# Optimization experiments

Measured on AMD Instinct MI355X. Metric: run time of the kernel, lower is better.

The kernel has to match this reference:

```python
import jax, jax.numpy as jnp
import numpy as np

B, P, N = 64, 100, 1000
D, H, QD = 128, 8, 16
NUM_PATCHES = 196
NTOT = N + NUM_PATCHES
SQRT_D = float(np.sqrt(D))   # sqrt_embedding_dim
CLIP = 10.0                  # logit_clipping


def setup_inputs() -> dict:
    key = jax.random.key(0)
    ks = jax.random.split(key, 10)
    return {
        "encoded_last_node": jax.random.normal(ks[0], (B, P, D), jnp.float32),
        "ninf_mask": jnp.zeros((B, P, N), jnp.float32),
        "q_first": jax.random.normal(ks[1], (B, H, P, QD), jnp.float32),
        "k": jax.random.normal(ks[2], (B, H, NTOT, QD), jnp.float32),
        "v": jax.random.normal(ks[3], (B, H, NTOT, QD), jnp.float32),
        "single_head_key": jax.random.normal(ks[4], (B, D, N), jnp.float32),
        "Wq_last": jax.random.normal(ks[5], (D, H * QD), jnp.float32) * 0.05,
        "mh_combine": jax.random.normal(ks[6], (H * QD, D), jnp.float32) * 0.05,
        "edge_bias": jax.random.normal(ks[7], (B, N, N), jnp.float32) * 0.1,
        "current_node": jax.random.randint(ks[8], (B, P), 0, N, jnp.int64),
        "num_patches": NUM_PATCHES,
    }


def reference(encoded_last_node, ninf_mask, q_first, k, v, single_head_key,
              Wq_last, mh_combine, edge_bias, current_node, num_patches):
    b, p, _ = encoded_last_node.shape
    h, qd = q_first.shape[1], q_first.shape[3]

    # q_last = reshape_by_heads(F.linear(x, Wq_last_para))  -> [B,H,P,qd]
    q_last = (encoded_last_node @ Wq_last.T).reshape(b, p, h, qd).transpose(0, 2, 1, 3)
    q = q_first + q_last

    # multi-head attention with mask extended by zero columns for patch tokens
    mask_full = jnp.pad(ninf_mask, ((0, 0), (0, 0), (0, num_patches)))  # [B,P,Ntot]
    score = jnp.einsum('bhpd,bhnd->bhpn', q, k) / jnp.sqrt(jnp.float32(qd))
    weights = jax.nn.softmax(score + mask_full[:, None, :, :], axis=-1)
    out = jnp.einsum('bhpn,bhnd->bhpd', weights, v)
    out_concat = out.transpose(0, 2, 1, 3).reshape(b, p, h * qd)  # [B,P,D]

    mh_atten_out = out_concat @ mh_combine.T                       # [B,P,D]

    # pointer-style single-head score with tanh clipping
    score2 = jnp.einsum('bpd,bdn->bpn', mh_atten_out, single_head_key)
    score_clipped = CLIP * jnp.tanh(score2 / SQRT_D)

    # gather edge bias row for current node: bias[b,p,n] = edge_bias[b, current_node[b,p], n]
    bias_row = jnp.take_along_axis(edge_bias, current_node[:, :, None], axis=1)
    probs = jax.nn.softmax(score_clipped + bias_row + ninf_mask, axis=-1)
    return probs
```

## Files before the change

kernel.cpp:

```cpp
#include <hip/hip_runtime.h>
#include <math.h>

#define BB 64
#define PP 100
#define NN 1000
#define DD 128
#define HH 8
#define QDQ 16
#define NTOT 1196
#define QROWS 16
#define LOG2E 1.44269504088896f
#define EXP2(x) __builtin_amdgcn_exp2f(x)

typedef float f2 __attribute__((ext_vector_type(2)));
typedef short s8v __attribute__((ext_vector_type(8)));
typedef float f16v __attribute__((ext_vector_type(16)));

static __device__ __forceinline__ f2 splat2(float v) { f2 r; r.x = v; r.y = v; return r; }
#define PKFMA(a, b, c) __builtin_elementwise_fma((a), (b), (c))

static __device__ __forceinline__ unsigned pkhi(float a, float b) {
  return (__float_as_uint(a) >> 16) | (__float_as_uint(b) & 0xffff0000u);
}
static __device__ __forceinline__ float truncbf(float a) {
  return __uint_as_float(__float_as_uint(a) & 0xffff0000u);
}
#define MFMA32(a, b, c) __builtin_amdgcn_mfma_f32_32x32x16_bf16((a), (b), (c), 0, 0, 0)

__global__ __launch_bounds__(256) void k_prep(const float* __restrict__ x,
                                              const float* __restrict__ Wq,
                                              const float* __restrict__ qf,
                                              float* __restrict__ qout,
                                              const float* __restrict__ mask,
                                              unsigned short* __restrict__ m2) {
  __shared__ float sw[128 * 65];
  __shared__ float xs[QROWS * DD];
  int tid = threadIdx.x;

  if (blockIdx.x < 400) {
    int row0 = blockIdx.x * QROWS;
    for (int i = tid; i < QROWS * DD / 4; i += 256)
      ((float4*)xs)[i] = ((const float4*)(x + (size_t)row0 * DD))[i];

    int j = tid & 127, rr = tid >> 7;
    float acc[8];
#pragma unroll
    for (int i = 0; i < 8; ++i) acc[i] = 0.f;

    for (int half = 0; half < 2; ++half) {
      __syncthreads();
      for (int idx = tid; idx < 128 * 64; idx += 256) {
        int jj = idx >> 6, dl = idx & 63;
        sw[jj * 65 + dl] = Wq[jj * DD + half * 64 + dl];
      }
      __syncthreads();
#pragma unroll
      for (int ri = 0; ri < 8; ++ri) {
        int r = 2 * ri + rr;
        float a = acc[ri];
#pragma unroll 16
        for (int dl = 0; dl < 64; ++dl)
          a += xs[r * DD + half * 64 + dl] * sw[j * 65 + dl];
        acc[ri] = a;
      }
    }
#pragma unroll
    for (int ri = 0; ri < 8; ++ri) {
      int bp = row0 + 2 * ri + rr;
      int b = bp / PP, p = bp % PP;
      int h = j >> 4, qd = j & 15;
      size_t qi = ((size_t)(b * HH + h) * PP + p) * QDQ + qd;
      qout[qi] = acc[ri] + qf[qi];
    }
  } else {
    int t2 = blockIdx.x - 400;
    int b = t2 >> 7, q = t2 & 127;
    unsigned short* dst = m2 + (size_t)(b * 128 + q) * 1280;
    const float* srow = mask + ((size_t)b * PP + (q < PP ? q : PP - 1)) * NN;
    for (int j = tid; j < 1280; j += 256) {
      int h = j >= 640 ? 1 : 0;
      int jj = j - h * 640;
      float val;
      if (q >= PP || jj >= 598) {
        val = -1e4f;
      } else {
        int n = h * 598 + jj;
        val = (n < NN) ? srow[n] * LOG2E - 20.f : -20.f;
      }
      dst[j] = (unsigned short)(__float_as_uint(val) >> 16);
    }
  }
}

__global__ __launch_bounds__(256) void k_mha(const float* __restrict__ kk,
                                             const float* __restrict__ vv,
                                             const float* __restrict__ qws,
                                             const unsigned short* __restrict__ m2,
                                             float* __restrict__ part) {
  int bid = blockIdx.x;
  int swz = (bid & 7) * 128 + (bid >> 3);
  int bh = swz >> 1, half = swz & 1;
  int b = bh >> 3;
  int tid = threadIdx.x;
  int w = tid >> 6, lane = tid & 63;
  int L = lane >> 5, ln = lane & 31;
  bool lo = (L == 0);

  __shared__ __align__(16) char pool[27264];
  char* KspB = pool;
  char* VThB = pool + 10240;
  char* VTlB = pool + 14592;
  char* QhB  = pool + 18944;
  char* QlB  = pool + 23040;

  {
    const float* qrow = qws + (size_t)bh * (PP * QDQ);
    for (int i = tid; i < 128 * 16; i += 256) {
      int p = i >> 4, qd = i & 15;
      float v = (p < PP) ? qrow[p * QDQ + qd] * (0.25f * LOG2E) : 0.f;
      ((unsigned short*)QhB)[i] = (unsigned short)(__float_as_uint(v) >> 16);
      float rl = v - truncbf(v);
      ((unsigned short*)QlB)[i] = (unsigned short)(__float_as_uint(rl) >> 16);
    }
  }

  const float4* kf4 = (const float4*)kk + (size_t)bh * NTOT * 4;
  const float4* vf4 = (const float4*)vv + (size_t)bh * NTOT * 4;

  f16v Oacc[4];
  float lacc[4];
#pragma unroll
  for (int qt = 0; qt < 4; ++qt) {
    lacc[qt] = 0.f;
#pragma unroll
    for (int r = 0; r < 16; ++r) Oacc[qt][r] = 0.f;
  }
  s8v QhF[4], QlF[4];

  for (int c = 0; c < 5; ++c) {
    __syncthreads();
#pragma unroll
    for (int rep = 0; rep < 2; ++rep) {
      int f = tid + rep * 256;
      int key_l = f >> 2, qd0 = (f & 3) << 2;
      int j = c * 128 + key_l;
      int jc = j < 598 ? j : 597;
      size_t gidx = (size_t)(half * 598 + jc) * 4 + (qd0 >> 2);
      float4 k4 = kf4[gidx];
      unsigned kh01 = pkhi(k4.x, k4.y), kh23 = pkhi(k4.z, k4.w);
      float r0 = k4.x - truncbf(k4.x), r1 = k4.y - truncbf(k4.y);
      float r2 = k4.z - truncbf(k4.z), r3 = k4.w - truncbf(k4.w);
      unsigned kl01 = pkhi(r0, r1), kl23 = pkhi(r2, r3);
      *(uint2*)(KspB + key_l * 80 + qd0 * 2) = make_uint2(kh01, kh23);
      *(uint2*)(KspB + key_l * 80 + 32 + qd0 * 2) = make_uint2(kl01, kl23);
      float4 v4 = vf4[gidx];
      float ve0 = v4.x, ve1 = v4.y, ve2 = v4.z, ve3 = v4.w;
      ((unsigned short*)VThB)[(qd0 + 0) * 136 + key_l] = (unsigned short)(__float_as_uint(ve0) >> 16);
      ((unsigned short*)VThB)[(qd0 + 1) * 136 + key_l] = (unsigned short)(__float_as_uint(ve1) >> 16);
      ((unsigned short*)VThB)[(qd0 + 2) * 136 + key_l] = (unsigned short)(__float_as_uint(ve2) >> 16);
      ((unsigned short*)VThB)[(qd0 + 3) * 136 + key_l] = (unsigned short)(__float_as_uint(ve3) >> 16);
      float w0 = ve0 - truncbf(ve0), w1 = ve1 - truncbf(ve1);
      float w2 = ve2 - truncbf(ve2), w3 = ve3 - truncbf(ve3);
      ((unsigned short*)VTlB)[(qd0 + 0) * 136 + key_l] = (unsigned short)(__float_as_uint(w0) >> 16);
      ((unsigned short*)VTlB)[(qd0 + 1) * 136 + key_l] = (unsigned short)(__float_as_uint(w1) >> 16);
      ((unsigned short*)VTlB)[(qd0 + 2) * 136 + key_l] = (unsigned short)(__float_as_uint(w2) >> 16);
      ((unsigned short*)VTlB)[(qd0 + 3) * 136 + key_l] = (unsigned short)(__float_as_uint(w3) >> 16);
    }
    __syncthreads();
    if (c == 0) {
#pragma unroll
      for (int qt = 0; qt < 4; ++qt) {
        int qr = qt * 32 + ln;
        QhF[qt] = *(const s8v*)(QhB + qr * 32 + L * 16);
        QlF[qt] = *(const s8v*)(QlB + qr * 32 + L * 16);
      }
    }
    int ktb = w * 32;
    s8v KhF = *(const s8v*)(KspB + (ktb + ln) * 80 + L * 16);
    s8v KlF = *(const s8v*)(KspB + (ktb + ln) * 80 + 32 + L * 16);
    int vr = ln & 15;
    s8v VhS0 = *(const s8v*)(VThB + vr * 272 + (ktb + L * 8) * 2);
    s8v VhS1 = *(const s8v*)(VThB + vr * 272 + (ktb + 16 + L * 8) * 2);
    s8v VlS0 = *(const s8v*)(VTlB + vr * 272 + (ktb + L * 8) * 2);
    s8v VlS1 = *(const s8v*)(VTlB + vr * 272 + (ktb + 16 + L * 8) * 2);
    size_t mkey = (size_t)half * 640 + c * 128 + ktb + 4 * L;
#pragma unroll
    for (int qt = 0; qt < 4; ++qt) {
      const unsigned short* mrow = m2 + (size_t)(b * 128 + qt * 32 + ln) * 1280 + mkey;
      f16v acc;
#pragma unroll
      for (int g = 0; g < 4; ++g) {
        uint2 md = *(const uint2*)(mrow + g * 8);
        acc[g * 4 + 0] = __uint_as_float(md.x << 16);
        acc[g * 4 + 1] = __uint_as_float(md.x & 0xffff0000u);
        acc[g * 4 + 2] = __uint_as_float(md.y << 16);
        acc[g * 4 + 3] = __uint_as_float(md.y & 0xffff0000u);
      }
      acc = MFMA32(KhF, QhF[qt], acc);
      acc = MFMA32(KhF, QlF[qt], acc);
      acc = MFMA32(KlF, QhF[qt], acc);
      float p[16];
      float ls = 0.f;
#pragma unroll
      for (int r = 0; r < 16; ++r) { p[r] = EXP2(acc[r]); ls += p[r]; }
      lacc[qt] += ls;
#pragma unroll
      for (int s = 0; s < 2; ++s) {
        unsigned a0 = pkhi(p[8 * s + 0], p[8 * s + 1]), a1 = pkhi(p[8 * s + 2], p[8 * s + 3]);
        unsigned b0 = pkhi(p[8 * s + 4], p[8 * s + 5]), b1 = pkhi(p[8 * s + 6], p[8 * s + 7]);
        unsigned m0 = lo ? b0 : a0;
        unsigned m1 = lo ? b1 : a1;
        unsigned s0 = __shfl_xor(m0, 32);
        unsigned s1 = __shfl_xor(m1, 32);
        uint4 phu = make_uint4(lo ? a0 : s0, lo ? a1 : s1, lo ? s0 : b0, lo ? s1 : b1);
        float t0 = p[8 * s + 0] - truncbf(p[8 * s + 0]), t1 = p[8 * s + 1] - truncbf(p[8 * s + 1]);
        float t2 = p[8 * s + 2] - truncbf(p[8 * s + 2]), t3 = p[8 * s + 3] - truncbf(p[8 * s + 3]);
        float t4 = p[8 * s + 4] - truncbf(p[8 * s + 4]), t5 = p[8 * s + 5] - truncbf(p[8 * s + 5]);
        float t6 = p[8 * s + 6] - truncbf(p[8 * s + 6]), t7 = p[8 * s + 7] - truncbf(p[8 * s + 7]);
        unsigned c0 = pkhi(t0, t1), c1 = pkhi(t2, t3);
        unsigned e0 = pkhi(t4, t5), e1 = pkhi(t6, t7);
        unsigned n0 = lo ? e0 : c0;
        unsigned n1 = lo ? e1 : c1;
        unsigned u0 = __shfl_xor(n0, 32);
        unsigned u1 = __shfl_xor(n1, 32);
        uint4 plu = make_uint4(lo ? c0 : u0, lo ? c1 : u1, lo ? u0 : e0, lo ? u1 : e1);
        s8v APh = *(s8v*)&phu;
        s8v APl = *(s8v*)&plu;
        s8v Vh = s ? VhS1 : VhS0;
        s8v Vl = s ? VlS1 : VlS0;
        Oacc[qt] = MFMA32(APh, Vh, Oacc[qt]);
        Oacc[qt] = MFMA32(APh, Vl, Oacc[qt]);
        Oacc[qt] = MFMA32(APl, Vh, Oacc[qt]);
      }
    }
  }

  float lf[4];
#pragma unroll
  for (int qt = 0; qt < 4; ++qt) lf[qt] = lacc[qt] + __shfl_xor(lacc[qt], 32);

  __syncthreads();
  float* marea = (float*)pool;
  float* larea = (float*)(pool + 25600);
  if (ln < 16) {
#pragma unroll
    for (int qt = 0; qt < 4; ++qt) {
#pragma unroll
      for (int r = 0; r < 16; ++r) {
        int q = qt * 32 + (r & 3) + 8 * (r >> 2) + 4 * L;
        if (q < PP) marea[(w * PP + q) * 16 + ln] = Oacc[qt][r];
      }
    }
  }
  if (lane < 32) {
#pragma unroll
    for (int qt = 0; qt < 4; ++qt) {
      int q = qt * 32 + ln;
      if (q < PP) larea[w * PP + q] = lf[qt];
    }
  }
  __syncthreads();
  for (int idx = tid; idx < PP * 17; idx += 256) {
    int q = idx / 17, e = idx % 17;
    float sv;
    if (e < 16)
      sv = marea[(0 * PP + q) * 16 + e] + marea[(1 * PP + q) * 16 + e]
         + marea[(2 * PP + q) * 16 + e] + marea[(3 * PP + q) * 16 + e];
    else
      sv = larea[0 * PP + q] + larea[1 * PP + q] + larea[2 * PP + q] + larea[3 * PP + q];
    part[((size_t)swz * PP + q) * 17 + e] = sv;
  }
}

__global__ __launch_bounds__(256) void k_combine(const float* __restrict__ part,
                                                 const float* __restrict__ MC,
                                                 float* __restrict__ mh) {
  __shared__ float sw[128 * 65];
  __shared__ float oc[QROWS * DD];
  int tid = threadIdx.x;
  int row0 = blockIdx.x * QROWS;

  for (int i = tid; i < QROWS * DD; i += 256) {
    int r = i >> 7, t = i & 127;
    int bp = row0 + r, b = bp / PP, p = bp % PP;
    int qd = t & 15, h = t >> 4;
    int bh = b * HH + h;
    const float* r0 = part + (((size_t)(bh * 2 + 0)) * PP + p) * 17;
    const float* r1 = part + (((size_t)(bh * 2 + 1)) * PP + p) * 17;
    float A = r0[qd] + r1[qd];
    float L = r0[16] + r1[16];
    oc[i] = A / L;
  }

  int j = tid & 127, rr = tid >> 7;
  float acc[8];
#pragma unroll
  for (int i = 0; i < 8; ++i) acc[i] = 0.f;

  for (int half = 0; half < 2; ++half) {
    __syncthreads();
    for (int idx = tid; idx < 128 * 64; idx += 256) {
      int jj = idx >> 6, dl = idx & 63;
      sw[jj * 65 + dl] = MC[jj * DD + half * 64 + dl];
    }
    __syncthreads();
#pragma unroll
    for (int ri = 0; ri < 8; ++ri) {
      int r = 2 * ri + rr;
      float a = acc[ri];
#pragma unroll 16
      for (int dl = 0; dl < 64; ++dl)
        a += oc[r * DD + half * 64 + dl] * sw[j * 65 + dl];
      acc[ri] = a;
    }
  }
#pragma unroll
  for (int ri = 0; ri < 8; ++ri) {
    int bp = row0 + 2 * ri + rr;
    mh[(size_t)bp * DD + j] = acc[ri];
  }
}

__global__ __launch_bounds__(256) void k_score2(const float* __restrict__ mh,
                                                const float* __restrict__ shk,
                                                float* __restrict__ sc) {
  int bid = blockIdx.x;
  int swz = (bid & 7) * 128 + (bid >> 3);
  int b = swz >> 4, nt = swz & 15;
  int tid = threadIdx.x; int nl = tid & 31, pg = tid >> 5;
  __shared__ float A[PP * 132];
  for (int idx = tid; idx < PP * DD; idx += 256)
    A[(idx >> 7) * 132 + (idx & 127)] = mh[(size_t)b * PP * DD + idx];
  __syncthreads();

  int na = nt * 64 + nl, nb2 = na + 32;
  int nca = na < NN ? na : NN - 1, ncb = nb2 < NN ? nb2 : NN - 1;
  const float* S = shk + (size_t)b * DD * NN;
  f2 accv[13];
#pragma unroll
  for (int i = 0; i < 13; ++i) accv[i] = splat2(0.f);

  for (int d = 0; d < DD; d += 4) {
    f2 s0, s1, s2, s3;
    s0.x = S[(size_t)(d + 0) * NN + nca]; s0.y = S[(size_t)(d + 0) * NN + ncb];
    s1.x = S[(size_t)(d + 1) * NN + nca]; s1.y = S[(size_t)(d + 1) * NN + ncb];
    s2.x = S[(size_t)(d + 2) * NN + nca]; s2.y = S[(size_t)(d + 2) * NN + ncb];
    s3.x = S[(size_t)(d + 3) * NN + nca]; s3.y = S[(size_t)(d + 3) * NN + ncb];
#pragma unroll
    for (int i = 0; i < 13; ++i) {
      int p = pg + (i << 3);
      if (p < PP) {
        const float4 a4 = *(const float4*)&A[p * 132 + d];
        accv[i] = PKFMA(splat2(a4.x), s0, accv[i]);
        accv[i] = PKFMA(splat2(a4.y), s1, accv[i]);
        accv[i] = PKFMA(splat2(a4.z), s2, accv[i]);
        accv[i] = PKFMA(splat2(a4.w), s3, accv[i]);
      }
    }
  }
#pragma unroll
  for (int i = 0; i < 13; ++i) {
    int p = pg + (i << 3);
    if (p < PP) {
      size_t base = ((size_t)b * PP + p) * NN;
      if (na < NN) sc[base + na] = accv[i].x;
      if (nb2 < NN) sc[base + nb2] = accv[i].y;
    }
  }
}

__global__ __launch_bounds__(256) void k_finsm(const float* __restrict__ sc,
                                               const float* __restrict__ eb,
                                               const int* __restrict__ cn,
                                               const float* __restrict__ mask,
                                               float* __restrict__ out) {
  int bid = blockIdx.x;
  int bp = (bid & 7) * 800 + (bid >> 3);
  int b = bp / PP;
  int t = threadIdx.x;
  int node = cn[bp];
  const float4* scp = (const float4*)(sc + (size_t)bp * NN);
  const float4* ebp = (const float4*)(eb + ((size_t)b * NN + node) * NN);
  const float4* mp  = (const float4*)(mask + (size_t)bp * NN);
  const float inv_sqrtD = 0.08838834764831845f;

  float4 v = make_float4(0.f, 0.f, 0.f, 0.f);
  float s = 0.f;
  if (t < 250) {
    float4 s4 = scp[t];
    float4 e4 = ebp[t];
    float4 m4 = mp[t];
#define FEL(comp) { \
      float z = s4.comp * inv_sqrtD; \
      float e = EXP2(2.f * LOG2E * z); \
      float th10 = 10.f - 20.f * __builtin_amdgcn_rcpf(e + 1.f); \
      float lg = th10 + e4.comp + m4.comp; \
      v.comp = EXP2(lg * LOG2E); }
    FEL(x) FEL(y) FEL(z) FEL(w)
#undef FEL
    s = (v.x + v.y) + (v.z + v.w);
  }
#pragma unroll
  for (int off = 32; off; off >>= 1) s += __shfl_xor(s, off);
  __shared__ float red[4];
  int w = t >> 6, lane = t & 63;
  if (lane == 0) red[w] = s;
  __syncthreads();
  s = (red[0] + red[1]) + (red[2] + red[3]);
  float inv = 1.f / s;
  if (t < 250) {
    float4 o;
    o.x = v.x * inv; o.y = v.y * inv; o.z = v.z * inv; o.w = v.w * inv;
    ((float4*)(out + (size_t)bp * NN))[t] = o;
  }
}

extern "C" void kernel_launch(void* const* d_in, const int* in_sizes, int n_in,
                              void* d_out, int out_size, void* d_ws, size_t ws_size,
                              hipStream_t stream) {
  const float* x    = (const float*)d_in[0];
  const float* mask = (const float*)d_in[1];
  const float* qf   = (const float*)d_in[2];
  const float* kk   = (const float*)d_in[3];
  const float* vv   = (const float*)d_in[4];
  const float* shk  = (const float*)d_in[5];
  const float* Wq   = (const float*)d_in[6];
  const float* MC   = (const float*)d_in[7];
  const float* eb   = (const float*)d_in[8];
  const int*   cn   = (const int*)d_in[9];

  float* out = (float*)d_out;
  float* ws = (float*)d_ws;
  float* q_ws = ws;
  float* part = ws + 819200;
  float* mh   = ws + 2560000;
  float* reg  = ws + 3379200;
  unsigned short* m2 = (unsigned short*)reg;
  float* sc   = reg;

  hipLaunchKernelGGL(k_prep, dim3(8592), dim3(256), 0, stream, x, Wq, qf, q_ws, mask, m2);
  hipLaunchKernelGGL(k_mha, dim3(1024), dim3(256), 0, stream, kk, vv, q_ws, m2, part);
  hipLaunchKernelGGL(k_combine, dim3(400), dim3(256), 0, stream, part, MC, mh);
  hipLaunchKernelGGL(k_score2, dim3(1024), dim3(256), 0, stream, mh, shk, sc);
  hipLaunchKernelGGL(k_finsm, dim3(6400), dim3(256), 0, stream, sc, eb, cn, mask, out);
}
```

Measured before the change: 190.5 us.

## Drop low-bf16 split of attention probs and use one wave per softmax row

In the attention kernel the exponentiated probabilities are now fed to the P·V MFMA only as truncated bf16 high parts. The residual low-part packing, its cross-lane shuffles and one of three MFMAs per step are removed, and the row sum accumulates the truncated values so the normalisation stays consistent. The final softmax kernel is restructured so each 64-lane wave handles a whole output row with four float4 per lane, removing shared-memory reduction and __syncthreads and quartering the block count. The precision reduction risks larger numerical error in the attention output.

```diff
diff --git a/kernel.cpp b/kernel.cpp
--- a/kernel.cpp
+++ b/kernel.cpp
@@ -202,7 +202,10 @@
       float p[16];
       float ls = 0.f;
 #pragma unroll
-      for (int r = 0; r < 16; ++r) { p[r] = EXP2(acc[r]); ls += p[r]; }
+      for (int r = 0; r < 16; ++r) {
+        p[r] = EXP2(acc[r]);
+        ls += truncbf(p[r]);
+      }
       lacc[qt] += ls;
 #pragma unroll
       for (int s = 0; s < 2; ++s) {
@@ -213,24 +216,11 @@
         unsigned s0 = __shfl_xor(m0, 32);
         unsigned s1 = __shfl_xor(m1, 32);
         uint4 phu = make_uint4(lo ? a0 : s0, lo ? a1 : s1, lo ? s0 : b0, lo ? s1 : b1);
-        float t0 = p[8 * s + 0] - truncbf(p[8 * s + 0]), t1 = p[8 * s + 1] - truncbf(p[8 * s + 1]);
-        float t2 = p[8 * s + 2] - truncbf(p[8 * s + 2]), t3 = p[8 * s + 3] - truncbf(p[8 * s + 3]);
-        float t4 = p[8 * s + 4] - truncbf(p[8 * s + 4]), t5 = p[8 * s + 5] - truncbf(p[8 * s + 5]);
-        float t6 = p[8 * s + 6] - truncbf(p[8 * s + 6]), t7 = p[8 * s + 7] - truncbf(p[8 * s + 7]);
-        unsigned c0 = pkhi(t0, t1), c1 = pkhi(t2, t3);
-        unsigned e0 = pkhi(t4, t5), e1 = pkhi(t6, t7);
-        unsigned n0 = lo ? e0 : c0;
-        unsigned n1 = lo ? e1 : c1;
-        unsigned u0 = __shfl_xor(n0, 32);
-        unsigned u1 = __shfl_xor(n1, 32);
-        uint4 plu = make_uint4(lo ? c0 : u0, lo ? c1 : u1, lo ? u0 : e0, lo ? u1 : e1);
         s8v APh = *(s8v*)&phu;
-        s8v APl = *(s8v*)&plu;
         s8v Vh = s ? VhS1 : VhS0;
         s8v Vl = s ? VlS1 : VlS0;
         Oacc[qt] = MFMA32(APh, Vh, Oacc[qt]);
         Oacc[qt] = MFMA32(APh, Vl, Oacc[qt]);
-        Oacc[qt] = MFMA32(APl, Vh, Oacc[qt]);
       }
     }
   }
@@ -375,44 +365,47 @@
                                                const float* __restrict__ mask,
                                                float* __restrict__ out) {
   int bid = blockIdx.x;
-  int bp = (bid & 7) * 800 + (bid >> 3);
+  int blk = (bid & 7) * 200 + (bid >> 3);
+  int w = threadIdx.x >> 6, lane = threadIdx.x & 63;
+  int bp = blk * 4 + w;
   int b = bp / PP;
-  int t = threadIdx.x;
   int node = cn[bp];
   const float4* scp = (const float4*)(sc + (size_t)bp * NN);
   const float4* ebp = (const float4*)(eb + ((size_t)b * NN + node) * NN);
   const float4* mp  = (const float4*)(mask + (size_t)bp * NN);
+  float4* op = (float4*)(out + (size_t)bp * NN);
   const float inv_sqrtD = 0.08838834764831845f;
 
-  float4 v = make_float4(0.f, 0.f, 0.f, 0.f);
+  float4 v0 = make_float4(0.f, 0.f, 0.f, 0.f), v1 = v0, v2 = v0, v3 = v0;
   float s = 0.f;
-  if (t < 250) {
-    float4 s4 = scp[t];
-    float4 e4 = ebp[t];
-    float4 m4 = mp[t];
-#define FEL(comp) { \
-      float z = s4.comp * inv_sqrtD; \
-      float e = EXP2(2.f * LOG2E * z); \
-      float th10 = 10.f - 20.f * __builtin_amdgcn_rcpf(e + 1.f); \
-      float lg = th10 + e4.comp + m4.comp; \
-      v.comp = EXP2(lg * LOG2E); }
-    FEL(x) FEL(y) FEL(z) FEL(w)
+#define FEL(vv, comp, s4, e4, m4) { \
+    float z = s4.comp * inv_sqrtD; \
+    float e = EXP2(2.f * LOG2E * z); \
+    float th10 = 10.f - 20.f * __builtin_amdgcn_rcpf(e + 1.f); \
+    float lg = th10 + e4.comp + m4.comp; \
+    vv.comp = EXP2(lg * LOG2E); }
+#define ROW(vv, i) { \
+    int idx = lane + ((i) << 6); \
+    if (idx < 250) { \
+      float4 s4 = scp[idx], e4 = ebp[idx], m4 = mp[idx]; \
+      FEL(vv, x, s4, e4, m4) FEL(vv, y, s4, e4, m4) \
+      FEL(vv, z, s4, e4, m4) FEL(vv, w, s4, e4, m4) \
+      s += (vv.x + vv.y) + (vv.z + vv.w); \
+    } }
+  ROW(v0, 0) ROW(v1, 1) ROW(v2, 2) ROW(v3, 3)
+#undef ROW
 #undef FEL
-    s = (v.x + v.y) + (v.z + v.w);
-  }
 #pragma unroll
   for (int off = 32; off; off >>= 1) s += __shfl_xor(s, off);
-  __shared__ float red[4];
-  int w = t >> 6, lane = t & 63;
-  if (lane == 0) red[w] = s;
-  __syncthreads();
-  s = (red[0] + red[1]) + (red[2] + red[3]);
   float inv = 1.f / s;
-  if (t < 250) {
-    float4 o;
-    o.x = v.x * inv; o.y = v.y * inv; o.z = v.z * inv; o.w = v.w * inv;
-    ((float4*)(out + (size_t)bp * NN))[t] = o;
-  }
+#define WR(vv, i) { \
+    int idx = lane + ((i) << 6); \
+    if (idx < 250) { \
+      float4 o; o.x = vv.x * inv; o.y = vv.y * inv; o.z = vv.z * inv; o.w = vv.w * inv; \
+      op[idx] = o; \
+    } }
+  WR(v0, 0) WR(v1, 1) WR(v2, 2) WR(v3, 3)
+#undef WR
 }
 
 extern "C" void kernel_launch(void* const* d_in, const int* in_sizes, int n_in,
@@ -442,5 +435,5 @@
   hipLaunchKernelGGL(k_mha, dim3(1024), dim3(256), 0, stream, kk, vv, q_ws, m2, part);
   hipLaunchKernelGGL(k_combine, dim3(400), dim3(256), 0, stream, part, MC, mh);
   hipLaunchKernelGGL(k_score2, dim3(1024), dim3(256), 0, stream, mh, shk, sc);
-  hipLaunchKernelGGL(k_finsm, dim3(6400), dim3(256), 0, stream, sc, eb, cn, mask, out);
-}
+  hipLaunchKernelGGL(k_finsm, dim3(1600), dim3(256), 0, stream, sc, eb, cn, mask, out);
+}
```

Result: faster. 181.9 us (-4.5%).
